# Performance work log

Measured on AMD Instinct MI355X. Metric: run time of the kernel, lower is better.

Reference implementation:

```python
import jax, jax.numpy as jnp
import numpy as np

N = 50000      # nodes per graph
E = 800000     # directed edges per graph
L = 64         # number_of_labels
F1, F2, F3 = 64, 64, 32
K = 16         # tensor_neurons


def setup_inputs() -> dict:
    key = jax.random.key(0)
    ks = jax.random.split(key, 16)
    def glorot(k, shape):
        fan_in, fan_out = shape[0], shape[-1]
        s = (6.0 / (fan_in + fan_out)) ** 0.5
        return jax.random.uniform(k, shape, jnp.float32, -s, s)
    return {
        "features_1": jax.random.normal(ks[0], (N, L), jnp.float32),
        "edge_index_1": jax.random.randint(ks[1], (2, E), 0, N, jnp.int64 if jax.config.jax_enable_x64 else jnp.int32),
        "features_2": jax.random.normal(ks[2], (N, L), jnp.float32),
        "edge_index_2": jax.random.randint(ks[3], (2, E), 0, N, jnp.int64 if jax.config.jax_enable_x64 else jnp.int32),
        "W1": glorot(ks[4], (L, F1)),  "b1": jnp.zeros((F1,), jnp.float32),
        "W2": glorot(ks[5], (F1, F2)), "b2": jnp.zeros((F2,), jnp.float32),
        "W3": glorot(ks[6], (F2, F3)), "b3": jnp.zeros((F3,), jnp.float32),
        "W_att": glorot(ks[7], (F3, F3)),
        "W_tn": glorot(ks[8], (F3, F3, K)),        # NTN bilinear tensor
        "W_block": glorot(ks[9], (K, 2 * F3)),      # NTN linear block
        "b_tn": jnp.zeros((K, 1), jnp.float32),
        "index": 0,
    }


def _gcn(x, edge_index, W, b):
    # PyG GCNConv: add self-loops, symmetric normalization, scatter-add.
    n = x.shape[0]
    loop = jnp.arange(n, dtype=edge_index.dtype)
    src = jnp.concatenate([edge_index[0], loop])
    dst = jnp.concatenate([edge_index[1], loop])
    deg = jax.ops.segment_sum(jnp.ones_like(dst, dtype=x.dtype), dst, num_segments=n)
    dinv = jnp.where(deg > 0, deg ** -0.5, 0.0)
    norm = dinv[src] * dinv[dst]                 # [E+n]
    h = x @ W                                    # [n, F_out]
    out = jax.ops.segment_sum(h[src] * norm[:, None], dst, num_segments=n)
    return out + b


def _conv_pass(edge_index, x, W1, b1, W2, b2, W3, b3):
    x = jax.nn.relu(_gcn(x, edge_index, W1, b1))   # dropout p=0 (eval)
    x = jax.nn.relu(_gcn(x, edge_index, W2, b2))
    return _gcn(x, edge_index, W3, b3)


def _att_pool(x, W_att):
    # SimGNN attention: tanh of mean-transformed global context, sigmoid scores.
    ctx = jnp.tanh(jnp.mean(x @ W_att, axis=0))    # [F3]
    sc = jax.nn.sigmoid(x @ ctx)                   # [N]
    return x.T @ sc[:, None]                       # [F3, 1]


def _ntn(e1, e2, W_tn, W_block, b_tn):
    f3 = e1.shape[0]
    scoring = (e1.T @ W_tn.reshape(f3, -1)).reshape(f3, -1)  # [F3, K]
    scoring = scoring.T @ e2                                  # [K, 1]
    block = W_block @ jnp.concatenate([e1, e2], axis=0)       # [K, 1]
    return jax.nn.relu(scoring + block + b_tn)


def reference(features_1, edge_index_1, features_2, edge_index_2,
              W1, b1, W2, b2, W3, b3, W_att, W_tn, W_block, b_tn, index):
    a1 = _conv_pass(edge_index_1, features_1, W1, b1, W2, b2, W3, b3)
    a2 = _conv_pass(edge_index_2, features_2, W1, b1, W2, b2, W3, b3)
    p1 = _att_pool(a1, W_att)
    p2 = _att_pool(a2, W_att)   # `index` unused (no source for forward_2 variant)
    scores = _ntn(p1, p2, W_tn, W_block, b_tn)     # [K, 1]
    return scores.T                                 # [1, K]
```

## Files before the change

kernel.cpp:

```cpp
#include <hip/hip_runtime.h>
#include <math.h>


#define NSLICE 64
#define NBLK   256

typedef _Float16 f16x8 __attribute__((ext_vector_type(8)));
typedef _Float16 f16x4 __attribute__((ext_vector_type(4)));
typedef _Float16 f16x2 __attribute__((ext_vector_type(2)));
typedef float    f32x4 __attribute__((ext_vector_type(4)));

__global__ void bcount_kernel(const int* __restrict__ ei1, const int* __restrict__ ei2,
                              int E, int N, int* __restrict__ gcnt, int chunk, int nsb) {
    __shared__ int cnt[NSLICE];
    int t = threadIdx.x;
    if (t < NSLICE) cnt[t] = 0;
    __syncthreads();
    int E2 = 2 * E;
    int lo = blockIdx.x * chunk;
    int hi = lo + chunk; if (hi > E2) hi = E2;
    for (int i = lo + t; i < hi; i += blockDim.x) {
        int dst = (i < E) ? ei1[E + i] : (ei2[E + (i - E)] + N);
        atomicAdd(&cnt[dst >> nsb], 1);
    }
    __syncthreads();
    if (t < NSLICE) gcnt[t * NBLK + blockIdx.x] = cnt[t];
}

__global__ void bscan_kernel(int* __restrict__ gcnt, int* __restrict__ sliceStart,
                             int* __restrict__ row_ptr, int M, int E2) {
    __shared__ int sh[1024];
    int t = threadIdx.x;
    const int PER = (NSLICE * NBLK) / 1024;
    int base = t * PER;
    int vals[PER];
    int s = 0;
    #pragma unroll
    for (int k = 0; k < PER; ++k) { vals[k] = gcnt[base + k]; s += vals[k]; }
    sh[t] = s;
    __syncthreads();
    for (int off = 1; off < 1024; off <<= 1) {
        int v = (t >= off) ? sh[t - off] : 0;
        __syncthreads();
        sh[t] += v;
        __syncthreads();
    }
    int run = (t == 0) ? 0 : sh[t - 1];
    #pragma unroll
    for (int k = 0; k < PER; ++k) {
        gcnt[base + k] = run;
        run += vals[k];
    }
    __syncthreads();
    if (t < NSLICE) sliceStart[t] = gcnt[t * NBLK];
    if (t == 0) { sliceStart[NSLICE] = E2; row_ptr[M] = E2; }
}

__global__ void bwrite_kernel(const int* __restrict__ ei1, const int* __restrict__ ei2,
                              int E, int N, const int* __restrict__ gcnt,
                              unsigned* __restrict__ bkt, int chunk, int nsb) {
    __shared__ int cur[NSLICE];
    int t = threadIdx.x;
    if (t < NSLICE) cur[t] = gcnt[t * NBLK + blockIdx.x];
    __syncthreads();
    int E2 = 2 * E;
    unsigned mask = (1u << nsb) - 1u;
    int lo = blockIdx.x * chunk;
    int hi = lo + chunk; if (hi > E2) hi = E2;
    for (int i = lo + t; i < hi; i += blockDim.x) {
        int src, dst;
        if (i < E) { src = ei1[i];         dst = ei1[E + i]; }
        else       { src = ei2[i - E] + N; dst = ei2[E + (i - E)] + N; }
        int p = atomicAdd(&cur[dst >> nsb], 1);
        bkt[p] = ((unsigned)src << nsb) | ((unsigned)dst & mask);
    }
}

__global__ void fillC_fused_kernel(const unsigned* __restrict__ bkt,
                                   const int* __restrict__ sliceStart,
                                   int* __restrict__ row_ptr, float* __restrict__ dinv,
                                   int* __restrict__ col, int M, int nsb) {
    extern __shared__ int sm[];
    int nbins = 1 << nsb;
    unsigned mask = (unsigned)nbins - 1u;
    int* hist = sm;
    int* ssum = sm + nbins;
    int slice = blockIdx.x;
    int lo = slice << nsb;
    int t = threadIdx.x;
    for (int j = t; j < nbins; j += 1024) hist[j] = 0;
    __syncthreads();
    int s = sliceStart[slice], e = sliceStart[slice + 1];
    for (int i = s + t; i < e; i += 1024)
        atomicAdd(&hist[bkt[i] & mask], 1);
    __syncthreads();
    const int PER = nbins >> 10;
    int base = t * PER;
    int vals[4];
    int acc = 0;
    for (int k = 0; k < PER; ++k) { vals[k] = hist[base + k]; acc += vals[k]; }
    ssum[t] = acc;
    __syncthreads();
    for (int off = 1; off < 1024; off <<= 1) {
        int v = (t >= off) ? ssum[t - off] : 0;
        __syncthreads();
        ssum[t] += v;
        __syncthreads();
    }
    int run = s + ((t == 0) ? 0 : ssum[t - 1]);
    for (int k = 0; k < PER; ++k) {
        int idx = lo + base + k;
        if (idx < M) {
            row_ptr[idx] = run;
            dinv[idx] = rsqrtf((float)(vals[k] + 1));
        }
        hist[base + k] = run;
        run += vals[k];
    }
    __syncthreads();
    for (int i = s + t; i < e; i += 1024) {
        unsigned w = bkt[i];
        int p = atomicAdd(&hist[w & mask], 1);
        col[p] = (int)(w >> nsb);
    }
}

__global__ void scale0_kernel(const float* __restrict__ f1, const float* __restrict__ f2,
                              const float* __restrict__ dinv, _Float16* __restrict__ xs,
                              int n ) {
    int i4 = (blockIdx.x * blockDim.x + threadIdx.x) * 4;
    if (i4 >= 2 * n) return;
    const float* src = (i4 < n) ? (f1 + i4) : (f2 + (i4 - n));
    float dv = dinv[i4 >> 6];
    float4 v = *(const float4*)src;
    f16x4 o = { (_Float16)(v.x * dv), (_Float16)(v.y * dv),
                (_Float16)(v.z * dv), (_Float16)(v.w * dv) };
    *(f16x4*)(xs + i4) = o;
}

__global__ void packW_kernel(const float* __restrict__ W1, const float* __restrict__ W2,
                             const float* __restrict__ W3, _Float16* __restrict__ pk) {
    int t = blockIdx.x * blockDim.x + threadIdx.x;
    if (t < 8192) {
        const float* W = (t < 4096) ? W1 : W2;
        int idx = t & 4095;
        int j = idx & 7, slot = idx >> 3;
        int lane = slot & 63, s = (slot >> 6) & 1, ct = slot >> 7;
        int k = s * 32 + ((lane >> 4) << 3) + j;
        int n = ct * 16 + (lane & 15);
        pk[t] = (_Float16)W[k * 64 + n];
    } else if (t < 10240) {
        int idx = t - 8192;
        int j = idx & 7, slot = idx >> 3;
        int lane = slot & 63, s = (slot >> 6) & 1, ct = slot >> 7;
        int k = s * 32 + ((lane >> 4) << 3) + j;
        int n = ct * 16 + (lane & 15);
        pk[t] = (_Float16)W3[k * 32 + n];
    }
}

__global__ void agg64_kernel(const _Float16* __restrict__ xs, _Float16* __restrict__ out,
                             const int* __restrict__ row_ptr, const int* __restrict__ col,
                             const float* __restrict__ dinv, int N) {
    int g = blockIdx.x & 1;
    int nv = ((blockIdx.x >> 1) * blockDim.x + threadIdx.x) >> 4;
    int l = threadIdx.x & 15;
    if (nv >= N) return;
    int v = g * N + nv;
    const f16x4* row = (const f16x4*)(xs + (size_t)v * 64);
    f16x4 sv = row[l];
    float a0 = (float)sv[0], a1 = (float)sv[1], a2 = (float)sv[2], a3 = (float)sv[3];
    int s = row_ptr[v], e = row_ptr[v + 1];
    int i = s;
    for (; i + 8 <= e; i += 8) {
        int u0 = col[i],     u1 = col[i + 1], u2 = col[i + 2], u3 = col[i + 3];
        int u4 = col[i + 4], u5 = col[i + 5], u6 = col[i + 6], u7 = col[i + 7];
        f16x4 p0 = ((const f16x4*)(xs + (size_t)u0 * 64))[l];
        f16x4 p1 = ((const f16x4*)(xs + (size_t)u1 * 64))[l];
        f16x4 p2 = ((const f16x4*)(xs + (size_t)u2 * 64))[l];
        f16x4 p3 = ((const f16x4*)(xs + (size_t)u3 * 64))[l];
        f16x4 p4 = ((const f16x4*)(xs + (size_t)u4 * 64))[l];
        f16x4 p5 = ((const f16x4*)(xs + (size_t)u5 * 64))[l];
        f16x4 p6 = ((const f16x4*)(xs + (size_t)u6 * 64))[l];
        f16x4 p7 = ((const f16x4*)(xs + (size_t)u7 * 64))[l];
        a0 += (((float)p0[0] + (float)p1[0]) + ((float)p2[0] + (float)p3[0]))
            + (((float)p4[0] + (float)p5[0]) + ((float)p6[0] + (float)p7[0]));
        a1 += (((float)p0[1] + (float)p1[1]) + ((float)p2[1] + (float)p3[1]))
            + (((float)p4[1] + (float)p5[1]) + ((float)p6[1] + (float)p7[1]));
        a2 += (((float)p0[2] + (float)p1[2]) + ((float)p2[2] + (float)p3[2]))
            + (((float)p4[2] + (float)p5[2]) + ((float)p6[2] + (float)p7[2]));
        a3 += (((float)p0[3] + (float)p1[3]) + ((float)p2[3] + (float)p3[3]))
            + (((float)p4[3] + (float)p5[3]) + ((float)p6[3] + (float)p7[3]));
    }
    for (; i + 4 <= e; i += 4) {
        int u0 = col[i], u1 = col[i + 1], u2 = col[i + 2], u3 = col[i + 3];
        f16x4 p0 = ((const f16x4*)(xs + (size_t)u0 * 64))[l];
        f16x4 p1 = ((const f16x4*)(xs + (size_t)u1 * 64))[l];
        f16x4 p2 = ((const f16x4*)(xs + (size_t)u2 * 64))[l];
        f16x4 p3 = ((const f16x4*)(xs + (size_t)u3 * 64))[l];
        a0 += ((float)p0[0] + (float)p1[0]) + ((float)p2[0] + (float)p3[0]);
        a1 += ((float)p0[1] + (float)p1[1]) + ((float)p2[1] + (float)p3[1]);
        a2 += ((float)p0[2] + (float)p1[2]) + ((float)p2[2] + (float)p3[2]);
        a3 += ((float)p0[3] + (float)p1[3]) + ((float)p2[3] + (float)p3[3]);
    }
    for (; i < e; ++i) {
        f16x4 p = ((const f16x4*)(xs + (size_t)col[i] * 64))[l];
        a0 += (float)p[0]; a1 += (float)p[1]; a2 += (float)p[2]; a3 += (float)p[3];
    }
    float dv = dinv[v];
    f16x4 o = { (_Float16)(a0 * dv), (_Float16)(a1 * dv),
                (_Float16)(a2 * dv), (_Float16)(a3 * dv) };
    ((f16x4*)(out + (size_t)v * 64))[l] = o;
}

__global__ void mfma_gemm64_kernel(const _Float16* __restrict__ tA, _Float16* __restrict__ out,
                                   const _Float16* __restrict__ pk, const float* __restrict__ b1,
                                   const float* __restrict__ dinv, int M) {
    int wave = (blockIdx.x * blockDim.x + threadIdx.x) >> 6;
    int lane = threadIdx.x & 63;
    int base = wave * 16;
    if (base >= M) return;
    int l15 = lane & 15, q = lane >> 4;
    const f16x8* arow = (const f16x8*)(tA + (size_t)(base + l15) * 64);
    f16x8 a0 = arow[q];
    f16x8 a1 = arow[q + 4];
    const f16x8* bp = (const f16x8*)pk;
    f32x4 acc[4];
    #pragma unroll
    for (int ct = 0; ct < 4; ++ct) {
        f32x4 c = {0.f, 0.f, 0.f, 0.f};
        c = __builtin_amdgcn_mfma_f32_16x16x32_f16(a0, bp[(ct * 2 + 0) * 64 + lane], c, 0, 0, 0);
        c = __builtin_amdgcn_mfma_f32_16x16x32_f16(a1, bp[(ct * 2 + 1) * 64 + lane], c, 0, 0, 0);
        acc[ct] = c;
    }
    float dv[4];
    #pragma unroll
    for (int r = 0; r < 4; ++r) dv[r] = dinv[base + q * 4 + r];
    #pragma unroll
    for (int ct = 0; ct < 4; ++ct) {
        float bj = b1[ct * 16 + l15];
        #pragma unroll
        for (int r = 0; r < 4; ++r)
            out[(size_t)(base + q * 4 + r) * 64 + ct * 16 + l15] =
                (_Float16)(fmaxf(acc[ct][r] + bj, 0.f) * dv[r]);
    }
}

__global__ void mfma_gemm64_32_kernel(const _Float16* __restrict__ tA, _Float16* __restrict__ out,
                                      const _Float16* __restrict__ pk2, const _Float16* __restrict__ pk3,
                                      const float* __restrict__ b2, const float* __restrict__ dinv,
                                      int M) {
    __shared__ _Float16 xl[4][16][72];
    int wv = threadIdx.x >> 6;
    int wave = (blockIdx.x * blockDim.x + threadIdx.x) >> 6;
    int lane = threadIdx.x & 63;
    int base = wave * 16;
    if (base >= M) return;
    int l15 = lane & 15, q = lane >> 4;
    const f16x8* arow = (const f16x8*)(tA + (size_t)(base + l15) * 64);
    f16x8 a0 = arow[q];
    f16x8 a1 = arow[q + 4];
    const f16x8* bp2 = (const f16x8*)pk2;
    #pragma unroll
    for (int ct = 0; ct < 4; ++ct) {
        f32x4 c = {0.f, 0.f, 0.f, 0.f};
        c = __builtin_amdgcn_mfma_f32_16x16x32_f16(a0, bp2[(ct * 2 + 0) * 64 + lane], c, 0, 0, 0);
        c = __builtin_amdgcn_mfma_f32_16x16x32_f16(a1, bp2[(ct * 2 + 1) * 64 + lane], c, 0, 0, 0);
        float bj = b2[ct * 16 + l15];
        #pragma unroll
        for (int r = 0; r < 4; ++r)
            xl[wv][q * 4 + r][ct * 16 + l15] = (_Float16)fmaxf(c[r] + bj, 0.f);
    }
    const f16x8* xr = (const f16x8*)(&xl[wv][l15][0]);
    f16x8 e0 = xr[q];
    f16x8 e1 = xr[q + 4];
    const f16x8* bp3 = (const f16x8*)pk3;
    float dv[4];
    #pragma unroll
    for (int r = 0; r < 4; ++r) dv[r] = dinv[base + q * 4 + r];
    #pragma unroll
    for (int ct = 0; ct < 2; ++ct) {
        f32x4 c = {0.f, 0.f, 0.f, 0.f};
        c = __builtin_amdgcn_mfma_f32_16x16x32_f16(e0, bp3[(ct * 2 + 0) * 64 + lane], c, 0, 0, 0);
        c = __builtin_amdgcn_mfma_f32_16x16x32_f16(e1, bp3[(ct * 2 + 1) * 64 + lane], c, 0, 0, 0);
        #pragma unroll
        for (int r = 0; r < 4; ++r)
            out[(size_t)(base + q * 4 + r) * 32 + ct * 16 + l15] = (_Float16)(c[r] * dv[r]);
    }
}

__global__ void agg32_colsum_kernel(const _Float16* __restrict__ hs, float* __restrict__ out,
                                    const int* __restrict__ row_ptr, const int* __restrict__ col,
                                    const float* __restrict__ dinv, const float* __restrict__ b,
                                    float* __restrict__ msum, int N, int halfgrid) {
    int g = blockIdx.x & 1;
    int bid = blockIdx.x >> 1;
    int t = threadIdx.x;
    int l = t & 15;
    int qw = (bid * blockDim.x + t) >> 4;
    int nqw = (halfgrid * blockDim.x) >> 4;
    float blx = b[2 * l], bly = b[2 * l + 1];
    float csx = 0.f, csy = 0.f;
    int base = g * N;
    for (int vv = qw; vv < N; vv += nqw) {
        int v = base + vv;
        f16x2 sv = ((const f16x2*)(hs + (size_t)v * 32))[l];
        float ax = (float)sv.x, ay = (float)sv.y;
        int s = row_ptr[v], e = row_ptr[v + 1];
        int i = s;
        for (; i + 8 <= e; i += 8) {
            int u0 = col[i],     u1 = col[i + 1], u2 = col[i + 2], u3 = col[i + 3];
            int u4 = col[i + 4], u5 = col[i + 5], u6 = col[i + 6], u7 = col[i + 7];
            f16x2 p0 = ((const f16x2*)(hs + (size_t)u0 * 32))[l];
            f16x2 p1 = ((const f16x2*)(hs + (size_t)u1 * 32))[l];
            f16x2 p2 = ((const f16x2*)(hs + (size_t)u2 * 32))[l];
            f16x2 p3 = ((const f16x2*)(hs + (size_t)u3 * 32))[l];
            f16x2 p4 = ((const f16x2*)(hs + (size_t)u4 * 32))[l];
            f16x2 p5 = ((const f16x2*)(hs + (size_t)u5 * 32))[l];
            f16x2 p6 = ((const f16x2*)(hs + (size_t)u6 * 32))[l];
            f16x2 p7 = ((const f16x2*)(hs + (size_t)u7 * 32))[l];
            ax += (((float)p0.x + (float)p1.x) + ((float)p2.x + (float)p3.x))
                + (((float)p4.x + (float)p5.x) + ((float)p6.x + (float)p7.x));
            ay += (((float)p0.y + (float)p1.y) + ((float)p2.y + (float)p3.y))
                + (((float)p4.y + (float)p5.y) + ((float)p6.y + (float)p7.y));
        }
        for (; i + 4 <= e; i += 4) {
            int u0 = col[i], u1 = col[i + 1], u2 = col[i + 2], u3 = col[i + 3];
            f16x2 p0 = ((const f16x2*)(hs + (size_t)u0 * 32))[l];
            f16x2 p1 = ((const f16x2*)(hs + (size_t)u1 * 32))[l];
            f16x2 p2 = ((const f16x2*)(hs + (size_t)u2 * 32))[l];
            f16x2 p3 = ((const f16x2*)(hs + (size_t)u3 * 32))[l];
            ax += ((float)p0.x + (float)p1.x) + ((float)p2.x + (float)p3.x);
            ay += ((float)p0.y + (float)p1.y) + ((float)p2.y + (float)p3.y);
        }
        for (; i < e; ++i) {
            f16x2 p = ((const f16x2*)(hs + (size_t)col[i] * 32))[l];
            ax += (float)p.x; ay += (float)p.y;
        }
        float dv = dinv[v];
        float ox = ax * dv + blx, oy = ay * dv + bly;
        *(float2*)(out + (size_t)v * 32 + 2 * l) = make_float2(ox, oy);
        csx += ox; csy += oy;
    }
    __shared__ float spx[256], spy[256];
    spx[t] = csx; spy[t] = csy;
    __syncthreads();
    if (t < 16) {
        float sx = 0.f, sy = 0.f;
        for (int w = 0; w < 16; ++w) { sx += spx[w * 16 + t]; sy += spy[w * 16 + t]; }
        atomicAdd(&msum[g * 32 + 2 * t], sx);
        atomicAdd(&msum[g * 32 + 2 * t + 1], sy);
    }
}

__global__ void pool2_kernel(const float* __restrict__ a3, const float* __restrict__ msum,
                             const float* __restrict__ W_att, float* __restrict__ pooled,
                             int N, int halfgrid) {
    int g = (blockIdx.x >= halfgrid) ? 1 : 0;
    int bid = blockIdx.x - g * halfgrid;
    int t = threadIdx.x;
    int j = t & 31;
    float invN = 1.f / (float)N;
    float acc = 0.f;
    for (int i = 0; i < 32; ++i) acc += (msum[g * 32 + i] * invN) * W_att[i * 32 + j];
    float cj = tanhf(acc);
    int hw = (bid * blockDim.x + t) >> 5;
    int nhw = (halfgrid * blockDim.x) >> 5;
    const float* base = a3 + (size_t)g * N * 32;
    float local = 0.f;
    for (int n = hw; n < N; n += nhw) {
        float v = base[(size_t)n * 32 + j];
        float d = v * cj;
        #pragma unroll
        for (int off = 16; off; off >>= 1) d += __shfl_xor(d, off);
        float s = 1.f / (1.f + __expf(-d));
        local += s * v;
    }
    __shared__ float sp[256];
    sp[t] = local;
    __syncthreads();
    if (t < 32) {
        float s = 0.f;
        for (int w = 0; w < 8; ++w) s += sp[w * 32 + t];
        atomicAdd(&pooled[g * 32 + t], s);
    }
}

__global__ void ntn_kernel(const float* __restrict__ p1, const float* __restrict__ p2,
                           const float* __restrict__ W_tn, const float* __restrict__ W_block,
                           const float* __restrict__ b_tn, float* __restrict__ out) {
    int k = threadIdx.x;
    if (k >= 16) return;
    float sc = 0.f;
    for (int i = 0; i < 32; ++i) {
        float e1 = p1[i];
        for (int j = 0; j < 32; ++j) sc += e1 * W_tn[i * 512 + j * 16 + k] * p2[j];
    }
    float bl = 0.f;
    for (int j = 0; j < 32; ++j)
        bl += W_block[k * 64 + j] * p1[j] + W_block[k * 64 + 32 + j] * p2[j];
    float v = sc + bl + b_tn[k];
    out[k] = v > 0.f ? v : 0.f;
}

extern "C" void kernel_launch(void* const* d_in, const int* in_sizes, int n_in,
                              void* d_out, int out_size, void* d_ws, size_t ws_size,
                              hipStream_t stream) {
    const float* f1     = (const float*)d_in[0];
    const int*   ei1    = (const int*)  d_in[1];
    const float* f2     = (const float*)d_in[2];
    const int*   ei2    = (const int*)  d_in[3];
    const float* W1     = (const float*)d_in[4];
    const float* b1     = (const float*)d_in[5];
    const float* W2     = (const float*)d_in[6];
    const float* b2     = (const float*)d_in[7];
    const float* W3     = (const float*)d_in[8];
    const float* b3     = (const float*)d_in[9];
    const float* W_att  = (const float*)d_in[10];
    const float* W_tn   = (const float*)d_in[11];
    const float* W_blk  = (const float*)d_in[12];
    const float* b_tn   = (const float*)d_in[13];

    int N = in_sizes[0] / 64;
    int E = in_sizes[1] / 2;
    int M = 2 * N;
    int E2 = 2 * E;
    int nsb = 11;
    while ((NSLICE << nsb) < M) nsb++;

    char* ws = (char*)d_ws;
    size_t off = 0;
    auto alloc = [&](size_t bytes) -> void* {
        void* p = ws + off;
        off += (bytes + 511) & ~(size_t)511;
        return p;
    };
    _Float16*  xsA     = (_Float16*) alloc((size_t)M * 64 * sizeof(_Float16));
    _Float16*  xsB     = (_Float16*) alloc((size_t)M * 64 * sizeof(_Float16));
    _Float16*  tH      = (_Float16*) alloc((size_t)M * 64 * sizeof(_Float16));
    size_t a3_bytes  = (size_t)M * 32 * sizeof(float);
    size_t bkt_bytes = (size_t)E2 * sizeof(unsigned);
    char*  region    = (char*)alloc(a3_bytes > bkt_bytes ? a3_bytes : bkt_bytes);
    float*    a3  = (float*)region;
    unsigned* bkt = (unsigned*)region;
    int*       col     = (int*)      alloc((size_t)E2 * sizeof(int));
    int*       row_ptr = (int*)      alloc((size_t)(M + 1) * sizeof(int));
    float*     dinv    = (float*)    alloc((size_t)M * sizeof(float));
    int*       gcnt    = (int*)      alloc((size_t)NSLICE * NBLK * sizeof(int));
    int*       sliceSt = (int*)      alloc((NSLICE + 1) * sizeof(int));
    _Float16*  pk      = (_Float16*) alloc(10240 * sizeof(_Float16));
    float*     smalls  = (float*)    alloc(256 * sizeof(float));
    float* msum   = smalls;
    float* pooled = smalls + 64;
    _Float16* pk1 = pk, *pk2 = pk + 4096, *pk3 = pk + 8192;

    hipMemsetAsync(smalls, 0, 256 * sizeof(float), stream);

    int chunk = (E2 + NBLK - 1) / NBLK;
    int lds_fused = ((1 << nsb) + 1024) * sizeof(int);

    bcount_kernel<<<NBLK, 256, 0, stream>>>(ei1, ei2, E, N, gcnt, chunk, nsb);
    bscan_kernel<<<1, 1024, 0, stream>>>(gcnt, sliceSt, row_ptr, M, E2);
    bwrite_kernel<<<NBLK, 256, 0, stream>>>(ei1, ei2, E, N, gcnt, bkt, chunk, nsb);
    fillC_fused_kernel<<<NSLICE, 1024, lds_fused, stream>>>(bkt, sliceSt, row_ptr, dinv, col, M, nsb);

    packW_kernel<<<40, 256, 0, stream>>>(W1, W2, W3, pk);
    int cvb = (M * 64 / 4 + 255) / 256;
    scale0_kernel<<<cvb, 256, 0, stream>>>(f1, f2, dinv, xsA, N * 64);

    int nb64 = 2 * ((N * 16 + 255) / 256);
    int gw   = ((M / 16) + 3) / 4;
    agg64_kernel<<<nb64, 256, 0, stream>>>(xsA, tH, row_ptr, col, dinv, N);
    mfma_gemm64_kernel<<<gw, 256, 0, stream>>>(tH, xsB, pk1, b1, dinv, M);
    agg64_kernel<<<nb64, 256, 0, stream>>>(xsB, tH, row_ptr, col, dinv, N);
    mfma_gemm64_32_kernel<<<gw, 256, 0, stream>>>(tH, xsA, pk2, pk3, b2, dinv, M);

    const int HG = 512;
    agg32_colsum_kernel<<<2 * HG, 256, 0, stream>>>(xsA, a3, row_ptr, col, dinv, b3, msum, N, HG);

    pool2_kernel<<<2 * 256, 256, 0, stream>>>(a3, msum, W_att, pooled, N, 256);
    ntn_kernel<<<1, 64, 0, stream>>>(pooled, pooled + 32, W_tn, W_blk, b_tn, (float*)d_out);
}
```

Baseline: 335.8 us.

## Fuse neighbor aggregation with MFMA GEMM per 16-node tile via LDS

Merges each 64-wide aggregation kernel with the following MFMA GEMM kernel. A block of 256 threads gathers 16 node rows into shared memory, then four waves each compute one 16-column output tile. This removes the tH intermediate round trip through global memory and two kernel launches. The trade-off is a block barrier between the irregular gather and the GEMM, plus per-row bounds checks.

```diff
diff --git a/kernel.cpp b/kernel.cpp
--- a/kernel.cpp
+++ b/kernel.cpp
@@ -159,17 +159,13 @@
     }
 }
 
-__global__ void agg64_kernel(const _Float16* __restrict__ xs, _Float16* __restrict__ out,
-                             const int* __restrict__ row_ptr, const int* __restrict__ col,
-                             const float* __restrict__ dinv, int N) {
-    int g = blockIdx.x & 1;
-    int nv = ((blockIdx.x >> 1) * blockDim.x + threadIdx.x) >> 4;
-    int l = threadIdx.x & 15;
-    if (nv >= N) return;
-    int v = g * N + nv;
+__device__ inline void gather_row4(const _Float16* __restrict__ xs,
+                                   const int* __restrict__ row_ptr,
+                                   const int* __restrict__ col,
+                                   int v, int l, float a[4]) {
     const f16x4* row = (const f16x4*)(xs + (size_t)v * 64);
     f16x4 sv = row[l];
-    float a0 = (float)sv[0], a1 = (float)sv[1], a2 = (float)sv[2], a3 = (float)sv[3];
+    a[0] = (float)sv[0]; a[1] = (float)sv[1]; a[2] = (float)sv[2]; a[3] = (float)sv[3];
     int s = row_ptr[v], e = row_ptr[v + 1];
     int i = s;
     for (; i + 8 <= e; i += 8) {
@@ -183,14 +179,14 @@
         f16x4 p5 = ((const f16x4*)(xs + (size_t)u5 * 64))[l];
         f16x4 p6 = ((const f16x4*)(xs + (size_t)u6 * 64))[l];
         f16x4 p7 = ((const f16x4*)(xs + (size_t)u7 * 64))[l];
-        a0 += (((float)p0[0] + (float)p1[0]) + ((float)p2[0] + (float)p3[0]))
-            + (((float)p4[0] + (float)p5[0]) + ((float)p6[0] + (float)p7[0]));
-        a1 += (((float)p0[1] + (float)p1[1]) + ((float)p2[1] + (float)p3[1]))
-            + (((float)p4[1] + (float)p5[1]) + ((float)p6[1] + (float)p7[1]));
-        a2 += (((float)p0[2] + (float)p1[2]) + ((float)p2[2] + (float)p3[2]))
-            + (((float)p4[2] + (float)p5[2]) + ((float)p6[2] + (float)p7[2]));
-        a3 += (((float)p0[3] + (float)p1[3]) + ((float)p2[3] + (float)p3[3]))
-            + (((float)p4[3] + (float)p5[3]) + ((float)p6[3] + (float)p7[3]));
+        a[0] += (((float)p0[0] + (float)p1[0]) + ((float)p2[0] + (float)p3[0]))
+              + (((float)p4[0] + (float)p5[0]) + ((float)p6[0] + (float)p7[0]));
+        a[1] += (((float)p0[1] + (float)p1[1]) + ((float)p2[1] + (float)p3[1]))
+              + (((float)p4[1] + (float)p5[1]) + ((float)p6[1] + (float)p7[1]));
+        a[2] += (((float)p0[2] + (float)p1[2]) + ((float)p2[2] + (float)p3[2]))
+              + (((float)p4[2] + (float)p5[2]) + ((float)p6[2] + (float)p7[2]));
+        a[3] += (((float)p0[3] + (float)p1[3]) + ((float)p2[3] + (float)p3[3]))
+              + (((float)p4[3] + (float)p5[3]) + ((float)p6[3] + (float)p7[3]));
     }
     for (; i + 4 <= e; i += 4) {
         int u0 = col[i], u1 = col[i + 1], u2 = col[i + 2], u3 = col[i + 3];
@@ -198,94 +194,122 @@
         f16x4 p1 = ((const f16x4*)(xs + (size_t)u1 * 64))[l];
         f16x4 p2 = ((const f16x4*)(xs + (size_t)u2 * 64))[l];
         f16x4 p3 = ((const f16x4*)(xs + (size_t)u3 * 64))[l];
-        a0 += ((float)p0[0] + (float)p1[0]) + ((float)p2[0] + (float)p3[0]);
-        a1 += ((float)p0[1] + (float)p1[1]) + ((float)p2[1] + (float)p3[1]);
-        a2 += ((float)p0[2] + (float)p1[2]) + ((float)p2[2] + (float)p3[2]);
-        a3 += ((float)p0[3] + (float)p1[3]) + ((float)p2[3] + (float)p3[3]);
+        a[0] += ((float)p0[0] + (float)p1[0]) + ((float)p2[0] + (float)p3[0]);
+        a[1] += ((float)p0[1] + (float)p1[1]) + ((float)p2[1] + (float)p3[1]);
+        a[2] += ((float)p0[2] + (float)p1[2]) + ((float)p2[2] + (float)p3[2]);
+        a[3] += ((float)p0[3] + (float)p1[3]) + ((float)p2[3] + (float)p3[3]);
     }
     for (; i < e; ++i) {
         f16x4 p = ((const f16x4*)(xs + (size_t)col[i] * 64))[l];
-        a0 += (float)p[0]; a1 += (float)p[1]; a2 += (float)p[2]; a3 += (float)p[3];
-    }
-    float dv = dinv[v];
-    f16x4 o = { (_Float16)(a0 * dv), (_Float16)(a1 * dv),
-                (_Float16)(a2 * dv), (_Float16)(a3 * dv) };
-    ((f16x4*)(out + (size_t)v * 64))[l] = o;
-}
-
-__global__ void mfma_gemm64_kernel(const _Float16* __restrict__ tA, _Float16* __restrict__ out,
-                                   const _Float16* __restrict__ pk, const float* __restrict__ b1,
-                                   const float* __restrict__ dinv, int M) {
-    int wave = (blockIdx.x * blockDim.x + threadIdx.x) >> 6;
-    int lane = threadIdx.x & 63;
-    int base = wave * 16;
-    if (base >= M) return;
+        a[0] += (float)p[0]; a[1] += (float)p[1]; a[2] += (float)p[2]; a[3] += (float)p[3];
+    }
+}
+
+__global__ void agg_gemm1_kernel(const _Float16* __restrict__ xs, _Float16* __restrict__ out,
+                                 const int* __restrict__ row_ptr, const int* __restrict__ col,
+                                 const _Float16* __restrict__ pk, const float* __restrict__ b1,
+                                 const float* __restrict__ dinv, int N) {
+    __shared__ _Float16 xl[16][72];
+    int g = blockIdx.x & 1;
+    int tile = blockIdx.x >> 1;
+    int t = threadIdx.x;
+    int qw = t >> 4, l = t & 15;
+    int nv = tile * 16 + qw;
+    int v0 = g * N + tile * 16;
+    if (nv < N) {
+        int v = g * N + nv;
+        float a[4];
+        gather_row4(xs, row_ptr, col, v, l, a);
+        float dvv = dinv[v];
+        f16x4 o = { (_Float16)(a[0] * dvv), (_Float16)(a[1] * dvv),
+                    (_Float16)(a[2] * dvv), (_Float16)(a[3] * dvv) };
+        *(f16x4*)&xl[qw][l * 4] = o;
+    } else {
+        f16x4 z = { (_Float16)0.f, (_Float16)0.f, (_Float16)0.f, (_Float16)0.f };
+        *(f16x4*)&xl[qw][l * 4] = z;
+    }
+    __syncthreads();
+    int ct = t >> 6;
+    int lane = t & 63;
     int l15 = lane & 15, q = lane >> 4;
-    const f16x8* arow = (const f16x8*)(tA + (size_t)(base + l15) * 64);
+    const f16x8* arow = (const f16x8*)&xl[l15][0];
     f16x8 a0 = arow[q];
     f16x8 a1 = arow[q + 4];
     const f16x8* bp = (const f16x8*)pk;
-    f32x4 acc[4];
+    f32x4 c = {0.f, 0.f, 0.f, 0.f};
+    c = __builtin_amdgcn_mfma_f32_16x16x32_f16(a0, bp[(ct * 2 + 0) * 64 + lane], c, 0, 0, 0);
+    c = __builtin_amdgcn_mfma_f32_16x16x32_f16(a1, bp[(ct * 2 + 1) * 64 + lane], c, 0, 0, 0);
+    float bj = b1[ct * 16 + l15];
     #pragma unroll
-    for (int ct = 0; ct < 4; ++ct) {
-        f32x4 c = {0.f, 0.f, 0.f, 0.f};
-        c = __builtin_amdgcn_mfma_f32_16x16x32_f16(a0, bp[(ct * 2 + 0) * 64 + lane], c, 0, 0, 0);
-        c = __builtin_amdgcn_mfma_f32_16x16x32_f16(a1, bp[(ct * 2 + 1) * 64 + lane], c, 0, 0, 0);
-        acc[ct] = c;
-    }
-    float dv[4];
-    #pragma unroll
-    for (int r = 0; r < 4; ++r) dv[r] = dinv[base + q * 4 + r];
-    #pragma unroll
-    for (int ct = 0; ct < 4; ++ct) {
-        float bj = b1[ct * 16 + l15];
-        #pragma unroll
-        for (int r = 0; r < 4; ++r)
-            out[(size_t)(base + q * 4 + r) * 64 + ct * 16 + l15] =
-                (_Float16)(fmaxf(acc[ct][r] + bj, 0.f) * dv[r]);
-    }
-}
-
-__global__ void mfma_gemm64_32_kernel(const _Float16* __restrict__ tA, _Float16* __restrict__ out,
-                                      const _Float16* __restrict__ pk2, const _Float16* __restrict__ pk3,
-                                      const float* __restrict__ b2, const float* __restrict__ dinv,
-                                      int M) {
-    __shared__ _Float16 xl[4][16][72];
-    int wv = threadIdx.x >> 6;
-    int wave = (blockIdx.x * blockDim.x + threadIdx.x) >> 6;
-    int lane = threadIdx.x & 63;
-    int base = wave * 16;
-    if (base >= M) return;
+    for (int r = 0; r < 4; ++r) {
+        int nr = tile * 16 + q * 4 + r;
+        if (nr < N) {
+            int vr = v0 + q * 4 + r;
+            out[(size_t)vr * 64 + ct * 16 + l15] =
+                (_Float16)(fmaxf(c[r] + bj, 0.f) * dinv[vr]);
+        }
+    }
+}
+
+__global__ void agg_gemm2_kernel(const _Float16* __restrict__ xs, _Float16* __restrict__ out,
+                                 const int* __restrict__ row_ptr, const int* __restrict__ col,
+                                 const _Float16* __restrict__ pk2, const _Float16* __restrict__ pk3,
+                                 const float* __restrict__ b2, const float* __restrict__ dinv,
+                                 int N) {
+    __shared__ _Float16 xl[16][72];
+    __shared__ _Float16 x2[16][72];
+    int g = blockIdx.x & 1;
+    int tile = blockIdx.x >> 1;
+    int t = threadIdx.x;
+    int qw = t >> 4, l = t & 15;
+    int nv = tile * 16 + qw;
+    int v0 = g * N + tile * 16;
+    if (nv < N) {
+        int v = g * N + nv;
+        float a[4];
+        gather_row4(xs, row_ptr, col, v, l, a);
+        float dvv = dinv[v];
+        f16x4 o = { (_Float16)(a[0] * dvv), (_Float16)(a[1] * dvv),
+                    (_Float16)(a[2] * dvv), (_Float16)(a[3] * dvv) };
+        *(f16x4*)&xl[qw][l * 4] = o;
+    } else {
+        f16x4 z = { (_Float16)0.f, (_Float16)0.f, (_Float16)0.f, (_Float16)0.f };
+        *(f16x4*)&xl[qw][l * 4] = z;
+    }
+    __syncthreads();
+    int ct = t >> 6;
+    int lane = t & 63;
     int l15 = lane & 15, q = lane >> 4;
-    const f16x8* arow = (const f16x8*)(tA + (size_t)(base + l15) * 64);
-    f16x8 a0 = arow[q];
-    f16x8 a1 = arow[q + 4];
-    const f16x8* bp2 = (const f16x8*)pk2;
-    #pragma unroll
-    for (int ct = 0; ct < 4; ++ct) {
+    {
+        const f16x8* arow = (const f16x8*)&xl[l15][0];
+        f16x8 a0 = arow[q];
+        f16x8 a1 = arow[q + 4];
+        const f16x8* bp2 = (const f16x8*)pk2;
         f32x4 c = {0.f, 0.f, 0.f, 0.f};
         c = __builtin_amdgcn_mfma_f32_16x16x32_f16(a0, bp2[(ct * 2 + 0) * 64 + lane], c, 0, 0, 0);
         c = __builtin_amdgcn_mfma_f32_16x16x32_f16(a1, bp2[(ct * 2 + 1) * 64 + lane], c, 0, 0, 0);
         float bj = b2[ct * 16 + l15];
         #pragma unroll
         for (int r = 0; r < 4; ++r)
-            xl[wv][q * 4 + r][ct * 16 + l15] = (_Float16)fmaxf(c[r] + bj, 0.f);
-    }
-    const f16x8* xr = (const f16x8*)(&xl[wv][l15][0]);
-    f16x8 e0 = xr[q];
-    f16x8 e1 = xr[q + 4];
-    const f16x8* bp3 = (const f16x8*)pk3;
-    float dv[4];
-    #pragma unroll
-    for (int r = 0; r < 4; ++r) dv[r] = dinv[base + q * 4 + r];
-    #pragma unroll
-    for (int ct = 0; ct < 2; ++ct) {
+            x2[q * 4 + r][ct * 16 + l15] = (_Float16)fmaxf(c[r] + bj, 0.f);
+    }
+    __syncthreads();
+    if (ct < 2) {
+        const f16x8* er = (const f16x8*)&x2[l15][0];
+        f16x8 e0 = er[q];
+        f16x8 e1 = er[q + 4];
+        const f16x8* bp3 = (const f16x8*)pk3;
         f32x4 c = {0.f, 0.f, 0.f, 0.f};
         c = __builtin_amdgcn_mfma_f32_16x16x32_f16(e0, bp3[(ct * 2 + 0) * 64 + lane], c, 0, 0, 0);
         c = __builtin_amdgcn_mfma_f32_16x16x32_f16(e1, bp3[(ct * 2 + 1) * 64 + lane], c, 0, 0, 0);
         #pragma unroll
-        for (int r = 0; r < 4; ++r)
-            out[(size_t)(base + q * 4 + r) * 32 + ct * 16 + l15] = (_Float16)(c[r] * dv[r]);
+        for (int r = 0; r < 4; ++r) {
+            int nr = tile * 16 + q * 4 + r;
+            if (nr < N) {
+                int vr = v0 + q * 4 + r;
+                out[(size_t)vr * 32 + ct * 16 + l15] = (_Float16)(c[r] * dinv[vr]);
+            }
+        }
     }
 }
 
@@ -437,7 +461,6 @@
     };
     _Float16*  xsA     = (_Float16*) alloc((size_t)M * 64 * sizeof(_Float16));
     _Float16*  xsB     = (_Float16*) alloc((size_t)M * 64 * sizeof(_Float16));
-    _Float16*  tH      = (_Float16*) alloc((size_t)M * 64 * sizeof(_Float16));
     size_t a3_bytes  = (size_t)M * 32 * sizeof(float);
     size_t bkt_bytes = (size_t)E2 * sizeof(unsigned);
     char*  region    = (char*)alloc(a3_bytes > bkt_bytes ? a3_bytes : bkt_bytes);
@@ -468,12 +491,9 @@
     int cvb = (M * 64 / 4 + 255) / 256;
     scale0_kernel<<<cvb, 256, 0, stream>>>(f1, f2, dinv, xsA, N * 64);
 
-    int nb64 = 2 * ((N * 16 + 255) / 256);
-    int gw   = ((M / 16) + 3) / 4;
-    agg64_kernel<<<nb64, 256, 0, stream>>>(xsA, tH, row_ptr, col, dinv, N);
-    mfma_gemm64_kernel<<<gw, 256, 0, stream>>>(tH, xsB, pk1, b1, dinv, M);
-    agg64_kernel<<<nb64, 256, 0, stream>>>(xsB, tH, row_ptr, col, dinv, N);
-    mfma_gemm64_32_kernel<<<gw, 256, 0, stream>>>(tH, xsA, pk2, pk3, b2, dinv, M);
+    int nbg = 2 * ((N + 15) / 16);
+    agg_gemm1_kernel<<<nbg, 256, 0, stream>>>(xsA, xsB, row_ptr, col, pk1, b1, dinv, N);
+    agg_gemm2_kernel<<<nbg, 256, 0, stream>>>(xsB, xsA, row_ptr, col, pk2, pk3, b2, dinv, N);
 
     const int HG = 512;
     agg32_colsum_kernel<<<2 * HG, 256, 0, stream>>>(xsA, a3, row_ptr, col, dinv, b3, msum, N, HG);
```

After: 318.3 us. -5.2%, faster.
